# Kernel optimization log

Measured on AMD Instinct MI355X. Metric: run time of the kernel, lower is better.

## Reference

```python
import jax, jax.numpy as jnp
import numpy as np

N = 50000; E = 200000; H = 128; L = 3; T = 2; FOUT = 64
G = 1000; NP = 3; ATOM_V = 64; BOND_V = 8
EPS = 1e-5
_DEG_HIST = np.array([0., 50000., 75000., 50000., 25000.])
# PyG PNAConv: avg_deg['log'] = sum(hist[d] * log(d+1)) / num_nodes
AVG_DEG_LOG = float((np.log(np.arange(5) + 1.0) * _DEG_HIST).sum() / _DEG_HIST.sum())


def _bn(v, g, b):
    # training-mode BatchNorm1d (biased variance), eps=1e-5
    mu = v.mean(0)
    var = ((v - mu) ** 2).mean(0)
    return (v - mu) * jax.lax.rsqrt(var + EPS) * g + b


def setup_inputs() -> dict:
    key = jax.random.key(0)
    ks = jax.random.split(key, 16)
    def nrm(k, shape, fan):
        return (jax.random.normal(k, shape, dtype=jnp.float32) / np.sqrt(fan)).astype(jnp.float32)
    return {
        'x': jax.random.randint(ks[0], (N, 9), 0, ATOM_V),
        'edge_index': jax.random.randint(ks[1], (2, E), 0, N),
        'batch': jnp.sort(jax.random.randint(ks[2], (N,), 0, G)),
        'edge_attr_idx': jax.random.randint(ks[3], (E, 3), 0, BOND_V),
        'atom_emb': nrm(ks[4], (9, ATOM_V, H), H),
        'bond_emb': nrm(ks[5], (3, BOND_V, H), H),
        'edge_W': nrm(ks[6], (L, H, H), H), 'edge_b': jnp.zeros((L, H), jnp.float32),
        'pre_W': nrm(ks[7], (L, T, 3 * H, H), 3 * H), 'pre_b': jnp.zeros((L, T, H), jnp.float32),
        'post_W': nrm(ks[8], (L, T, 13 * H, FOUT), 13 * H), 'post_b': jnp.zeros((L, T, FOUT), jnp.float32),
        'lin_W': nrm(ks[9], (L, H, H), H), 'lin_b': jnp.zeros((L, H), jnp.float32),
        'bn_g': jnp.ones((L, H), jnp.float32), 'bn_b': jnp.zeros((L, H), jnp.float32),
        'mlp_W': nrm(ks[10], (2, H, H), H), 'mlp_b': jnp.zeros((2, H), jnp.float32),
        'mlp_g': jnp.ones((2, H), jnp.float32), 'mlp_be': jnp.zeros((2, H), jnp.float32),
        'hW1': nrm(ks[11], (H, H // 2), H), 'hb1': jnp.zeros((H // 2,), jnp.float32),
        'hg1': jnp.ones((H // 2,), jnp.float32), 'hbe1': jnp.zeros((H // 2,), jnp.float32),
        'hW2': nrm(ks[12], (H // 2, H // 4), H // 2), 'hb2': jnp.zeros((H // 4,), jnp.float32),
        'hg2': jnp.ones((H // 4,), jnp.float32), 'hbe2': jnp.zeros((H // 4,), jnp.float32),
        'hW3': nrm(ks[13], (H // 4, NP), H // 4), 'hb3': jnp.zeros((NP,), jnp.float32),
    }


def reference(x, edge_index, batch, edge_attr_idx, atom_emb, bond_emb,
              edge_W, edge_b, pre_W, pre_b, post_W, post_b, lin_W, lin_b,
              bn_g, bn_b, mlp_W, mlp_b, mlp_g, mlp_be,
              hW1, hb1, hg1, hbe1, hW2, hb2, hg2, hbe2, hW3, hb3):
    # encoders: sum of per-feature embeddings (OGB Atom/Bond encoder)
    h = atom_emb[jnp.arange(9), x].sum(1)               # [N,H]
    e = bond_emb[jnp.arange(3), edge_attr_idx].sum(1)   # [E,H]
    src, dst = edge_index[0], edge_index[1]
    cnt = jax.ops.segment_sum(jnp.ones((E,), jnp.float32), dst, N)
    deg = jnp.maximum(cnt, 1.0)[:, None, None]          # clamp(1), as in PyG scalers
    amp = jnp.log(deg + 1.0) / AVG_DEG_LOG
    att = AVG_DEG_LOG / jnp.log(deg + 1.0)
    has = (cnt > 0)[:, None, None]
    for l in range(L):
        ea = e @ edge_W[l] + edge_b[l]                                  # [E,H]
        msg_in = jnp.concatenate([h[dst], h[src], ea], -1)              # [E,3H]
        m = jnp.einsum('ef,tfh->eth', msg_in, pre_W[l]) + pre_b[l]      # [E,T,H]
        s1 = jax.ops.segment_sum(m, dst, N)
        s2 = jax.ops.segment_sum(m * m, dst, N)
        mean = s1 / deg
        std = jnp.sqrt(jax.nn.relu(s2 / deg - mean * mean) + EPS)
        mn = jnp.where(has, jax.ops.segment_min(m, dst, N), 0.0)
        mx = jnp.where(has, jax.ops.segment_max(m, dst, N), 0.0)
        agg = jnp.concatenate([mean, mn, mx, std], -1)                  # [N,T,4H]
        scaled = jnp.concatenate([agg, agg * amp, agg * att], -1)       # [N,T,12H]
        upd = jnp.concatenate(
            [jnp.broadcast_to(h[:, None, :], (N, T, H)), scaled], -1)   # [N,T,13H]
        o = jnp.einsum('ntf,tfo->nto', upd, post_W[l]) + post_b[l]      # [N,T,FOUT]
        o = o.reshape(N, T * FOUT) @ lin_W[l] + lin_b[l]                # [N,H]
        h = jax.nn.relu(_bn(o, bn_g[l], bn_b[l]))
    g = jax.ops.segment_sum(h, batch, G)                                # [G,H]
    for i in range(2):
        g = jax.nn.relu(_bn(g @ mlp_W[i] + mlp_b[i], mlp_g[i], mlp_be[i]))
    g = jax.nn.relu(_bn(g @ hW1 + hb1, hg1, hbe1))
    g = jax.nn.relu(_bn(g @ hW2 + hb2, hg2, hbe2))
    return g @ hW3 + hb3                                                # [G,NP]
```

## Files before the change

### kernel.cpp

```cpp
#include <hip/hip_runtime.h>
#include <math.h>


#define NN 50000
#define NE 200000
#define HD 128
#define NG 1000
#define EPSV 1e-5f
#define ALOGC 1.1330197327247628f

#define AP 1288
#define OPF 132
#define ECAP 512
#define SCB 49

typedef __bf16 bf16x8 __attribute__((ext_vector_type(8)));
typedef float f32x4 __attribute__((ext_vector_type(4)));

__device__ __forceinline__ unsigned short f2bf(float f) {
    unsigned int u = __float_as_uint(f);
    unsigned int r = (u + 0x7FFFu + ((u >> 16) & 1u)) >> 16;
    return (unsigned short)r;
}
__device__ __forceinline__ float bf2f(unsigned short h) {
    return __uint_as_float((unsigned int)h << 16);
}

__global__ void k_fill(float* __restrict__ o, float v, int n) {
    int i = blockIdx.x * 256 + threadIdx.x;
    if (i < n) o[i] = v;
}

__global__ void k_zero(float* __restrict__ z, int n) {
    int i = blockIdx.x * 256 + threadIdx.x;
    if (i < n) z[i] = 0.f;
}

__global__ __launch_bounds__(256) void k_encode_nodes(
    const int* __restrict__ x, const float* __restrict__ aemb, float* __restrict__ h) {
    __shared__ int xi[8][9];
    int nb = blockIdx.x * 8;
    int tid = threadIdx.x;
    if (tid < 72) xi[tid / 9][tid % 9] = x[nb * 9 + tid];
    __syncthreads();
    int node = tid >> 5, c4 = (tid & 31) * 4;
    float4 acc = make_float4(0.f, 0.f, 0.f, 0.f);
#pragma unroll
    for (int f = 0; f < 9; ++f) {
        float4 e = *(const float4*)(aemb + (size_t)(f * 64 + xi[node][f]) * HD + c4);
        acc.x += e.x; acc.y += e.y; acc.z += e.z; acc.w += e.w;
    }
    *(float4*)(h + (size_t)(nb + node) * HD + c4) = acc;
}

__global__ void k_count(const int* __restrict__ dst, int* __restrict__ cnt) {
    int e = blockIdx.x * 256 + threadIdx.x;
    if (e < NE) atomicAdd(&cnt[dst[e]], 1);
}

__global__ __launch_bounds__(1024) void k_scanA(const int* __restrict__ cnt,
                                                int* __restrict__ sc, int* __restrict__ tot) {
    __shared__ int buf[1024];
    int tid = threadIdx.x;
    int i = blockIdx.x * 1024 + tid;
    int v = (i < NN) ? cnt[i] : 0;
    buf[tid] = v;
    __syncthreads();
    for (int s = 1; s < 1024; s <<= 1) {
        int t = (tid >= s) ? buf[tid - s] : 0;
        __syncthreads();
        buf[tid] += t;
        __syncthreads();
    }
    if (i < NN) sc[i] = buf[tid];
    if (tid == 1023) tot[blockIdx.x] = buf[1023];
}

__global__ void k_scanB(const int* __restrict__ tot, int* __restrict__ offb) {
    if (threadIdx.x == 0) {
        int run = 0;
        for (int b = 0; b < SCB; ++b) { offb[b] = run; run += tot[b]; }
    }
}

__global__ __launch_bounds__(1024) void k_scanC(
    const int* __restrict__ cnt, const int* __restrict__ sc, const int* __restrict__ offb,
    int* __restrict__ rowptr, float* __restrict__ ampv, float* __restrict__ attv) {
    int i = blockIdx.x * 1024 + threadIdx.x;
    if (i == 0) rowptr[0] = 0;
    if (i < NN) {
        rowptr[i + 1] = offb[blockIdx.x] + sc[i];
        int v = cnt[i];
        float dg = (float)(v > 0 ? v : 1);
        float lg = logf(dg + 1.0f);
        ampv[i] = lg / ALOGC;
        attv[i] = ALOGC / lg;
    }
}

__global__ void k_scatter(const int* __restrict__ dst, const int* __restrict__ rowptr,
                          int* __restrict__ fill, int* __restrict__ eperm) {
    int e = blockIdx.x * 256 + threadIdx.x;
    if (e < NE) {
        int d = dst[e];
        int pos = rowptr[d] + atomicAdd(&fill[d], 1);
        eperm[pos] = e;
    }
}

__global__ void k_eprep(const int* __restrict__ ei, const int* __restrict__ eai,
                        const int* __restrict__ eperm, int* __restrict__ precs) {
    int p = blockIdx.x * 256 + threadIdx.x;
    if (p < NE) {
        int e = eperm[p];
        int cidx = eai[e * 3] | (eai[e * 3 + 1] << 3) | (eai[e * 3 + 2] << 6);
        precs[p] = ei[e] | (cidx << 17);
    }
}

__global__ void k_fold(const float* __restrict__ edge_W, const float* __restrict__ edge_b,
                       const float* __restrict__ pre_W, const float* __restrict__ pre_b,
                       float* __restrict__ cW, float* __restrict__ tb) {
    int l = blockIdx.y;
    int k = blockIdx.x;
    int tj = threadIdx.x;
    int t = tj >> 7, j = tj & 127;
    const float* pw = pre_W + ((size_t)(l * 2 + t) * 384 + 256) * 128 + j;
    if (k < 128) {
        const float* ew = edge_W + ((size_t)l * 128 + k) * 128;
        float acc = 0.f;
        for (int i = 0; i < 128; ++i) acc += ew[i] * pw[i * 128];
        cW[((size_t)l * 128 + k) * 256 + tj] = acc;
    } else {
        const float* eb = edge_b + l * 128;
        float acc = pre_b[(l * 2 + t) * 128 + j];
        for (int i = 0; i < 128; ++i) acc += eb[i] * pw[i * 128];
        tb[l * 256 + tj] = acc;
    }
}

__global__ void k_bond(const float* __restrict__ bemb, const float* __restrict__ cW,
                       float* __restrict__ bondc) {
    int v = blockIdx.x, f = blockIdx.y, l = blockIdx.z;
    int tj = threadIdx.x;
    const float* src = bemb + (size_t)(f * 8 + v) * 128;
    const float* w = cW + (size_t)l * 128 * 256;
    float acc = 0.f;
    for (int i = 0; i < 128; ++i) acc += src[i] * w[i * 256 + tj];
    bondc[(((size_t)l * 3 + f) * 8 + v) * 256 + tj] = acc;
}

__global__ void k_bcomb(const float* __restrict__ bondc, float* __restrict__ bcomb) {
    int ci = blockIdx.x, l = blockIdx.y, tj = threadIdx.x;
    const float* base = bondc + (size_t)l * 3 * 8 * 256;
    float v = base[((0 * 8) + (ci & 7)) * 256 + tj]
            + base[((1 * 8) + ((ci >> 3) & 7)) * 256 + tj]
            + base[((2 * 8) + (ci >> 6)) * 256 + tj];
    bcomb[((size_t)l * 512 + ci) * 256 + tj] = v;
}

__device__ __forceinline__ void pack_body2(const float* __restrict__ W, int N, int NT,
                                           unsigned short* __restrict__ pkh,
                                           unsigned short* __restrict__ pkl,
                                           int blk, int lane) {
    int kstep = blk / NT, nt = blk - kstep * NT;
    int kb = kstep * 32 + (lane >> 4) * 8;
    int col = nt * 16 + (lane & 15);
    unsigned short th[8], tl[8];
#pragma unroll
    for (int i = 0; i < 8; ++i) {
        float w = W[(size_t)(kb + i) * N + col];
        unsigned short hh = f2bf(w);
        th[i] = hh;
        tl[i] = f2bf(w - bf2f(hh));
    }
    size_t base = ((size_t)blk * 64 + lane) * 8;
    *(uint4*)(pkh + base) = *(uint4*)th;
    *(uint4*)(pkl + base) = *(uint4*)tl;
}

__global__ __launch_bounds__(64) void k_packall(
    const float* __restrict__ post_W, const float* __restrict__ lin_W,
    const float* __restrict__ pre_W,
    unsigned short* __restrict__ pkPostHi, unsigned short* __restrict__ pkPostLo,
    unsigned short* __restrict__ pkLinHi, unsigned short* __restrict__ pkLinLo,
    unsigned short* __restrict__ pkPreHi, unsigned short* __restrict__ pkPreLo) {
    int b = blockIdx.x;
    int lane = threadIdx.x;
    if (b < 1248) {
        int l = b / 416, rem = b % 416;
        int t = rem / 208, blk = rem % 208;
        size_t off = ((size_t)l * 2 + t) * 106496;
        pack_body2(post_W + ((size_t)l * 2 + t) * 1664 * 64, 64, 4,
                   pkPostHi + off, pkPostLo + off, blk, lane);
    } else if (b < 1344) {
        int idx = b - 1248;
        int l = idx / 32, blk = idx % 32;
        pack_body2(lin_W + (size_t)l * 128 * 128, 128, 8,
                   pkLinHi + (size_t)l * 16384, pkLinLo + (size_t)l * 16384, blk, lane);
    } else {
        int idx = b - 1344;
        int l = idx / 128, bb = idx % 128;
        const float* preW = pre_W + (size_t)l * 2 * 384 * 128;
        unsigned short* phi = pkPreHi + (size_t)l * 65536;
        unsigned short* plo = pkPreLo + (size_t)l * 65536;
        int kstep = bb >> 5, nt = bb & 31;
        int q = lane >> 4, nc = lane & 15;
        int col = nt * 16 + nc;
        int t = (col >> 7) & 1;
        int jcol = col & 127;
        int fbase = (col < 256) ? 0 : 128;
        unsigned short hi[8], lo[8];
#pragma unroll
        for (int i = 0; i < 8; ++i) {
            int k = kstep * 32 + q * 8 + i;
            float w = preW[((size_t)t * 384 + fbase + k) * 128 + jcol];
            unsigned short h16 = f2bf(w);
            hi[i] = h16;
            lo[i] = f2bf(w - bf2f(h16));
        }
        size_t base = ((size_t)bb * 64 + lane) * 8;
        *(uint4*)(phi + base) = *(uint4*)hi;
        *(uint4*)(plo + base) = *(uint4*)lo;
    }
}

__device__ __forceinline__ void pre_mfma_body(
    const unsigned short* __restrict__ ah, const unsigned short* __restrict__ al,
    const unsigned short* __restrict__ phi, const unsigned short* __restrict__ plo,
    const float* __restrict__ tb, int n0, int tid,
    float* __restrict__ hzd, float* __restrict__ hzs) {
    int lane = tid & 63, w = tid >> 6;
    int q = lane >> 4, nc = lane & 15;
    f32x4 acc[8];
#pragma unroll
    for (int j = 0; j < 8; ++j) acc[j] = (f32x4){0.f, 0.f, 0.f, 0.f};
#pragma unroll
    for (int kk = 0; kk < 4; ++kk) {
        bf16x8 Ahi = *(const bf16x8*)(ah + nc * 136 + kk * 32 + q * 8);
        bf16x8 Alo = *(const bf16x8*)(al + nc * 136 + kk * 32 + q * 8);
#pragma unroll
        for (int j = 0; j < 8; ++j) {
            int nt = w * 8 + j;
            size_t base = ((size_t)(kk * 32 + nt) * 64 + lane) * 8;
            bf16x8 Bhi = *(const bf16x8*)(phi + base);
            bf16x8 Blo = *(const bf16x8*)(plo + base);
            acc[j] = __builtin_amdgcn_mfma_f32_16x16x32_bf16(Ahi, Bhi, acc[j], 0, 0, 0);
            acc[j] = __builtin_amdgcn_mfma_f32_16x16x32_bf16(Ahi, Blo, acc[j], 0, 0, 0);
            acc[j] = __builtin_amdgcn_mfma_f32_16x16x32_bf16(Alo, Bhi, acc[j], 0, 0, 0);
        }
    }
#pragma unroll
    for (int j = 0; j < 8; ++j) {
        int col = (w * 8 + j) * 16 + nc;
#pragma unroll
        for (int reg = 0; reg < 4; ++reg) {
            int row = n0 + q * 4 + reg;
            if (col < 256) hzd[(size_t)row * 256 + col] = acc[j][reg] + tb[col];
            else           hzs[(size_t)row * 256 + (col - 256)] = acc[j][reg];
        }
    }
}

__global__ __launch_bounds__(256) void k_pre_m(
    const float* __restrict__ h,
    const unsigned short* __restrict__ phi, const unsigned short* __restrict__ plo,
    const float* __restrict__ tb,
    float* __restrict__ hzd, float* __restrict__ hzs) {
    __shared__ __align__(16) unsigned short ah[16 * 136];
    __shared__ __align__(16) unsigned short al[16 * 136];
    int n0 = blockIdx.x * 16;
    int tid = threadIdx.x;
    {
        int node = tid >> 4, cg = (tid & 15) * 8;
        const float* hs = h + (size_t)(n0 + node) * HD + cg;
        float4 v0 = *(const float4*)(hs);
        float4 v1 = *(const float4*)(hs + 4);
        float vv[8] = {v0.x, v0.y, v0.z, v0.w, v1.x, v1.y, v1.z, v1.w};
        unsigned short hh[8], ll[8];
#pragma unroll
        for (int i = 0; i < 8; ++i) {
            hh[i] = f2bf(vv[i]);
            ll[i] = f2bf(vv[i] - bf2f(hh[i]));
        }
        *(uint4*)(ah + node * 136 + cg) = *(uint4*)hh;
        *(uint4*)(al + node * 136 + cg) = *(uint4*)ll;
    }
    __syncthreads();
    pre_mfma_body(ah, al, phi, plo, tb, n0, tid, hzd, hzs);
}

__global__ __launch_bounds__(256) void k_bnpre(
    const float* __restrict__ o2, const float* __restrict__ stats,
    const float* __restrict__ g, const float* __restrict__ b,
    const unsigned short* __restrict__ phi, const unsigned short* __restrict__ plo,
    const float* __restrict__ tb,
    float* __restrict__ h, float* __restrict__ hzd, float* __restrict__ hzs) {
    __shared__ __align__(16) unsigned short ah[16 * 136];
    __shared__ __align__(16) unsigned short al[16 * 136];
    int n0 = blockIdx.x * 16;
    int tid = threadIdx.x;
    {
        int node = tid >> 4, cg = (tid & 15) * 8;
        int n = n0 + node;
        const float* os = o2 + (size_t)n * HD + cg;
        float4 v0 = *(const float4*)(os);
        float4 v1 = *(const float4*)(os + 4);
        float vv[8] = {v0.x, v0.y, v0.z, v0.w, v1.x, v1.y, v1.z, v1.w};
        unsigned short hh[8], ll[8];
        float ou[8];
#pragma unroll
        for (int i = 0; i < 8; ++i) {
            int c = cg + i;
            float mu = stats[c] * (1.f / NN);
            float var = stats[128 + c] * (1.f / NN) - mu * mu;
            float val = (vv[i] - mu) * rsqrtf(var + EPSV) * g[c] + b[c];
            val = fmaxf(val, 0.f);
            ou[i] = val;
            hh[i] = f2bf(val);
            ll[i] = f2bf(val - bf2f(hh[i]));
        }
        float* hd = h + (size_t)n * HD + cg;
        *(float4*)(hd) = make_float4(ou[0], ou[1], ou[2], ou[3]);
        *(float4*)(hd + 4) = make_float4(ou[4], ou[5], ou[6], ou[7]);
        *(uint4*)(ah + node * 136 + cg) = *(uint4*)hh;
        *(uint4*)(al + node * 136 + cg) = *(uint4*)ll;
    }
    __syncthreads();
    pre_mfma_body(ah, al, phi, plo, tb, n0, tid, hzd, hzs);
}

__global__ __launch_bounds__(256) void k_post(
    const float* __restrict__ h,
    const float* __restrict__ hzd, const float* __restrict__ hzs,
    const int* __restrict__ rowptr, const int* __restrict__ precs,
    const float* __restrict__ bcomb,
    const float* __restrict__ ampv, const float* __restrict__ attv,
    const unsigned short* __restrict__ pkPostHi, const unsigned short* __restrict__ pkPostLo,
    const float* __restrict__ postb,
    const unsigned short* __restrict__ pkLinHi, const unsigned short* __restrict__ pkLinLo,
    const float* __restrict__ linb,
    float* __restrict__ o2, float* __restrict__ stats) {
    __shared__ __align__(16) unsigned short a_lds[16 * AP];
    __shared__ __align__(16) float o_f[16 * OPF];
    __shared__ int es[ECAP];
    __shared__ float s_amp[16], s_att[16];
    int n0 = blockIdx.x * 16;
    int tid = threadIdx.x;

    int pbase = rowptr[n0];
    int ecount = rowptr[n0 + 16] - pbase;
    for (int i = tid; i < ecount && i < ECAP; i += 256) es[i] = precs[pbase + i];
    {
        int node = tid >> 4, cg = (tid & 15) * 8;
        const float* hs = h + (size_t)(n0 + node) * HD + cg;
        float4 v0 = *(const float4*)(hs);
        float4 v1 = *(const float4*)(hs + 4);
        unsigned short* d0 = a_lds + node * AP + cg;
        unsigned short* d1 = d0 + 640;
        unsigned short bb[8];
        bb[0] = f2bf(v0.x); bb[1] = f2bf(v0.y); bb[2] = f2bf(v0.z); bb[3] = f2bf(v0.w);
        bb[4] = f2bf(v1.x); bb[5] = f2bf(v1.y); bb[6] = f2bf(v1.z); bb[7] = f2bf(v1.w);
#pragma unroll
        for (int i = 0; i < 8; ++i) { d0[i] = bb[i]; d1[i] = bb[i]; }
    }
    if (tid < 16) { s_amp[tid] = ampv[n0 + tid]; s_att[tid] = attv[n0 + tid]; }
    __syncthreads();

    {
        int wv = tid >> 6, lane = tid & 63;
        int cc = lane * 4;
        int tt = cc >> 7, jj = cc & 127;
        bool incap = (ecount <= ECAP);
        const float4 Z4 = make_float4(0.f, 0.f, 0.f, 0.f);
        for (int i = 0; i < 4; ++i) {
            int r = wv * 4 + i;
            int n = n0 + r;
            int p0 = rowptr[n], p1 = rowptr[n + 1];
            float4 hd = *(const float4*)(hzd + (size_t)n * 256 + cc);
            float4 s1 = Z4, s2 = Z4;
            float4 mn = make_float4(3.4e38f, 3.4e38f, 3.4e38f, 3.4e38f);
            float4 mx = make_float4(-3.4e38f, -3.4e38f, -3.4e38f, -3.4e38f);
            for (int p = p0; p < p1; ++p) {
                int rec = incap ? es[p - pbase] : precs[p];
                int sp = rec & 131071;
                int ci = rec >> 17;
                float4 vs = *(const float4*)(hzs + (size_t)sp * 256 + cc);
                float4 bc = *(const float4*)(bcomb + (size_t)ci * 256 + cc);
                float wx = vs.x + bc.x, wy = vs.y + bc.y, wz = vs.z + bc.z, ww = vs.w + bc.w;
                s1.x += wx; s1.y += wy; s1.z += wz; s1.w += ww;
                s2.x += wx * wx; s2.y += wy * wy; s2.z += wz * wz; s2.w += ww * ww;
                mn.x = fminf(mn.x, wx); mn.y = fminf(mn.y, wy);
                mn.z = fminf(mn.z, wz); mn.w = fminf(mn.w, ww);
                mx.x = fmaxf(mx.x, wx); mx.y = fmaxf(mx.y, wy);
                mx.z = fmaxf(mx.z, wz); mx.w = fmaxf(mx.w, ww);
            }
            int cnt = p1 - p0;
            float inv = 1.f / (float)(cnt > 0 ? cnt : 1);
            float4 mw, stdv, mean;
            mw.x = s1.x * inv; mw.y = s1.y * inv; mw.z = s1.z * inv; mw.w = s1.w * inv;
            stdv.x = sqrtf(fmaxf(s2.x * inv - mw.x * mw.x, 0.f) + EPSV);
            stdv.y = sqrtf(fmaxf(s2.y * inv - mw.y * mw.y, 0.f) + EPSV);
            stdv.z = sqrtf(fmaxf(s2.z * inv - mw.z * mw.z, 0.f) + EPSV);
            stdv.w = sqrtf(fmaxf(s2.w * inv - mw.w * mw.w, 0.f) + EPSV);
            if (cnt > 0) {
                mean.x = hd.x + mw.x; mean.y = hd.y + mw.y;
                mean.z = hd.z + mw.z; mean.w = hd.w + mw.w;
                mn.x += hd.x; mn.y += hd.y; mn.z += hd.z; mn.w += hd.w;
                mx.x += hd.x; mx.y += hd.y; mx.z += hd.z; mx.w += hd.w;
            } else {
                mean = Z4; mn = Z4; mx = Z4;
            }
            unsigned short* d = a_lds + r * AP + tt * 640 + 128 + jj;
            d[0] = f2bf(mean.x); d[1] = f2bf(mean.y); d[2] = f2bf(mean.z); d[3] = f2bf(mean.w);
            d += 128; d[0] = f2bf(mn.x); d[1] = f2bf(mn.y); d[2] = f2bf(mn.z); d[3] = f2bf(mn.w);
            d += 128; d[0] = f2bf(mx.x); d[1] = f2bf(mx.y); d[2] = f2bf(mx.z); d[3] = f2bf(mx.w);
            d += 128; d[0] = f2bf(stdv.x); d[1] = f2bf(stdv.y); d[2] = f2bf(stdv.z); d[3] = f2bf(stdv.w);
        }
    }
    __syncthreads();

    {
        int lane = tid & 63;
        int w = tid >> 6;
        int t = w >> 1;
        int ntb = (w & 1) * 2;
        int q = lane >> 4, nc = lane & 15;
        const unsigned short* arow = a_lds + (size_t)nc * AP + t * 640 + q * 8;
        size_t toff = (size_t)t * 106496;
        const unsigned short* pkh = pkPostHi + toff;
        const unsigned short* pkl = pkPostLo + toff;
        f32x4 aP0 = {0.f, 0.f, 0.f, 0.f}, aP1 = {0.f, 0.f, 0.f, 0.f};
        f32x4 aA0 = {0.f, 0.f, 0.f, 0.f}, aA1 = {0.f, 0.f, 0.f, 0.f};
        f32x4 aT0 = {0.f, 0.f, 0.f, 0.f}, aT1 = {0.f, 0.f, 0.f, 0.f};
        for (int kk = 0; kk < 20; ++kk) {
            bf16x8 af = *(const bf16x8*)(arow + kk * 32);
            size_t ib = ((size_t)(kk * 4 + ntb) * 64 + lane) * 8;
            aP0 = __builtin_amdgcn_mfma_f32_16x16x32_bf16(af, *(const bf16x8*)(pkh + ib), aP0, 0, 0, 0);
            aP0 = __builtin_amdgcn_mfma_f32_16x16x32_bf16(af, *(const bf16x8*)(pkl + ib), aP0, 0, 0, 0);
            aP1 = __builtin_amdgcn_mfma_f32_16x16x32_bf16(af, *(const bf16x8*)(pkh + ib + 512), aP1, 0, 0, 0);
            aP1 = __builtin_amdgcn_mfma_f32_16x16x32_bf16(af, *(const bf16x8*)(pkl + ib + 512), aP1, 0, 0, 0);
            if (kk >= 4) {
                size_t ia = ((size_t)((kk + 16) * 4 + ntb) * 64 + lane) * 8;
                aA0 = __builtin_amdgcn_mfma_f32_16x16x32_bf16(af, *(const bf16x8*)(pkh + ia), aA0, 0, 0, 0);
                aA0 = __builtin_amdgcn_mfma_f32_16x16x32_bf16(af, *(const bf16x8*)(pkl + ia), aA0, 0, 0, 0);
                aA1 = __builtin_amdgcn_mfma_f32_16x16x32_bf16(af, *(const bf16x8*)(pkh + ia + 512), aA1, 0, 0, 0);
                aA1 = __builtin_amdgcn_mfma_f32_16x16x32_bf16(af, *(const bf16x8*)(pkl + ia + 512), aA1, 0, 0, 0);
                size_t it = ((size_t)((kk + 32) * 4 + ntb) * 64 + lane) * 8;
                aT0 = __builtin_amdgcn_mfma_f32_16x16x32_bf16(af, *(const bf16x8*)(pkh + it), aT0, 0, 0, 0);
                aT0 = __builtin_amdgcn_mfma_f32_16x16x32_bf16(af, *(const bf16x8*)(pkl + it), aT0, 0, 0, 0);
                aT1 = __builtin_amdgcn_mfma_f32_16x16x32_bf16(af, *(const bf16x8*)(pkh + it + 512), aT1, 0, 0, 0);
                aT1 = __builtin_amdgcn_mfma_f32_16x16x32_bf16(af, *(const bf16x8*)(pkl + it + 512), aT1, 0, 0, 0);
            }
        }
#pragma unroll
        for (int u = 0; u < 2; ++u) {
            int nt = ntb + u;
            int col = t * 64 + nt * 16 + nc;
            float pbia = postb[t * 64 + nt * 16 + nc];
            f32x4 P = u ? aP1 : aP0;
            f32x4 A = u ? aA1 : aA0;
            f32x4 T = u ? aT1 : aT0;
#pragma unroll
            for (int reg = 0; reg < 4; ++reg) {
                int mrow = q * 4 + reg;
                o_f[mrow * OPF + col] = P[reg] + s_amp[mrow] * A[reg] + s_att[mrow] * T[reg] + pbia;
            }
        }
    }
    __syncthreads();

    {
        int lane = tid & 63;
        int w = tid >> 6;
        int ntb = w * 2;
        int q = lane >> 4, nc = lane & 15;
        const float* arow = o_f + (size_t)nc * OPF + q * 8;
        f32x4 L0 = {0.f, 0.f, 0.f, 0.f}, L1 = {0.f, 0.f, 0.f, 0.f};
#pragma unroll
        for (int kk = 0; kk < 4; ++kk) {
            float4 a0 = *(const float4*)(arow + kk * 32);
            float4 a1 = *(const float4*)(arow + kk * 32 + 4);
            float vv[8] = {a0.x, a0.y, a0.z, a0.w, a1.x, a1.y, a1.z, a1.w};
            unsigned short hh[8], ll[8];
#pragma unroll
            for (int i = 0; i < 8; ++i) {
                hh[i] = f2bf(vv[i]);
                ll[i] = f2bf(vv[i] - bf2f(hh[i]));
            }
            bf16x8 Ahi = *(const bf16x8*)hh;
            bf16x8 Alo = *(const bf16x8*)ll;
            size_t ib = ((size_t)(kk * 8 + ntb) * 64 + lane) * 8;
            bf16x8 B0h = *(const bf16x8*)(pkLinHi + ib);
            bf16x8 B0l = *(const bf16x8*)(pkLinLo + ib);
            bf16x8 B1h = *(const bf16x8*)(pkLinHi + ib + 512);
            bf16x8 B1l = *(const bf16x8*)(pkLinLo + ib + 512);
            L0 = __builtin_amdgcn_mfma_f32_16x16x32_bf16(Ahi, B0h, L0, 0, 0, 0);
            L0 = __builtin_amdgcn_mfma_f32_16x16x32_bf16(Alo, B0h, L0, 0, 0, 0);
            L0 = __builtin_amdgcn_mfma_f32_16x16x32_bf16(Ahi, B0l, L0, 0, 0, 0);
            L1 = __builtin_amdgcn_mfma_f32_16x16x32_bf16(Ahi, B1h, L1, 0, 0, 0);
            L1 = __builtin_amdgcn_mfma_f32_16x16x32_bf16(Alo, B1h, L1, 0, 0, 0);
            L1 = __builtin_amdgcn_mfma_f32_16x16x32_bf16(Ahi, B1l, L1, 0, 0, 0);
        }
#pragma unroll
        for (int u = 0; u < 2; ++u) {
            int col = (ntb + u) * 16 + nc;
            float lb = linb[col];
            f32x4 L = u ? L1 : L0;
            float ps = 0.f, pss = 0.f;
#pragma unroll
            for (int reg = 0; reg < 4; ++reg) {
                int mrow = q * 4 + reg;
                float v = L[reg] + lb;
                o2[(size_t)(n0 + mrow) * HD + col] = v;
                ps += v; pss += v * v;
            }
            ps += __shfl_down(ps, 16); ps += __shfl_down(ps, 32);
            pss += __shfl_down(pss, 16); pss += __shfl_down(pss, 32);
            if (q == 0) {
                atomicAdd(&stats[col], ps);
                atomicAdd(&stats[128 + col], pss);
            }
        }
    }
}

__global__ void k_bn_relu(const float* __restrict__ o2, const float* __restrict__ stats,
                          const float* __restrict__ g, const float* __restrict__ b,
                          float* __restrict__ h) {
    int idx = blockIdx.x * 256 + threadIdx.x;
    int c = idx & 127;
    float mu = stats[c] * (1.f / NN);
    float var = stats[128 + c] * (1.f / NN) - mu * mu;
    float v = (o2[idx] - mu) * rsqrtf(var + EPSV) * g[c] + b[c];
    h[idx] = fmaxf(v, 0.f);
}

__global__ void k_pool(const float* __restrict__ h, const int* __restrict__ batch,
                       float* __restrict__ g0) {
    int c = threadIdx.x;
    int nbase = blockIdx.x * 64;
    float run = 0.f; int cur = -1;
    for (int i = 0; i < 64; ++i) {
        int n = nbase + i;
        if (n >= NN) break;
        int bb = batch[n];
        if (bb != cur) {
            if (cur >= 0) atomicAdd(&g0[(size_t)cur * HD + c], run);
            cur = bb; run = 0.f;
        }
        run += h[(size_t)n * HD + c];
    }
    if (cur >= 0) atomicAdd(&g0[(size_t)cur * HD + c], run);
}

__global__ void k_head_gemm(const float* __restrict__ x, const float* __restrict__ W,
                            const float* __restrict__ b, float* __restrict__ y,
                            float* __restrict__ stats, int K, int Kout) {
    int row = blockIdx.x;
    int col = threadIdx.x;
    if (col >= Kout) return;
    float acc = b[col];
    for (int k = 0; k < K; k += 4) {
        float4 xv = *(const float4*)(x + (size_t)row * K + k);
        acc += xv.x * W[(k + 0) * Kout + col] + xv.y * W[(k + 1) * Kout + col]
             + xv.z * W[(k + 2) * Kout + col] + xv.w * W[(k + 3) * Kout + col];
    }
    y[(size_t)row * Kout + col] = acc;
    if (stats) {
        atomicAdd(&stats[col], acc);
        atomicAdd(&stats[Kout + col], acc * acc);
    }
}

__global__ __launch_bounds__(128) void k_head_fused(
    const float* __restrict__ y_in, const float* __restrict__ stats_in,
    const float* __restrict__ g, const float* __restrict__ b,
    const float* __restrict__ W, const float* __restrict__ bias,
    float* __restrict__ y_out, float* __restrict__ stats_out, int Kin, int Kout) {
    __shared__ float row[128];
    int r = blockIdx.x, tid = threadIdx.x;
    if (tid < Kin) {
        float mu = stats_in[tid] * (1.f / NG);
        float var = stats_in[Kin + tid] * (1.f / NG) - mu * mu;
        float v = (y_in[(size_t)r * Kin + tid] - mu) * rsqrtf(var + EPSV) * g[tid] + b[tid];
        row[tid] = fmaxf(v, 0.f);
    }
    __syncthreads();
    if (tid < Kout) {
        float acc = bias[tid];
        for (int k = 0; k < Kin; ++k) acc += row[k] * W[(size_t)k * Kout + tid];
        y_out[(size_t)r * Kout + tid] = acc;
        if (stats_out) {
            atomicAdd(&stats_out[tid], acc);
            atomicAdd(&stats_out[Kout + tid], acc * acc);
        }
    }
}

extern "C" void kernel_launch(void* const* d_in, const int* in_sizes, int n_in,
                              void* d_out, int out_size, void* d_ws, size_t ws_size,
                              hipStream_t stream) {
    const int*   x        = (const int*)  d_in[0];
    const int*   ei       = (const int*)  d_in[1];
    const int*   batch    = (const int*)  d_in[2];
    const int*   eai      = (const int*)  d_in[3];
    const float* atom_emb = (const float*)d_in[4];
    const float* bond_emb = (const float*)d_in[5];
    const float* edge_W   = (const float*)d_in[6];
    const float* edge_b   = (const float*)d_in[7];
    const float* pre_W    = (const float*)d_in[8];
    const float* pre_b    = (const float*)d_in[9];
    const float* post_W   = (const float*)d_in[10];
    const float* post_b   = (const float*)d_in[11];
    const float* lin_W    = (const float*)d_in[12];
    const float* lin_b    = (const float*)d_in[13];
    const float* bn_g     = (const float*)d_in[14];
    const float* bn_b     = (const float*)d_in[15];
    const float* mlp_W    = (const float*)d_in[16];
    const float* mlp_b    = (const float*)d_in[17];
    const float* mlp_g    = (const float*)d_in[18];
    const float* mlp_be   = (const float*)d_in[19];
    const float* hW1 = (const float*)d_in[20]; const float* hb1  = (const float*)d_in[21];
    const float* hg1 = (const float*)d_in[22]; const float* hbe1 = (const float*)d_in[23];
    const float* hW2 = (const float*)d_in[24]; const float* hb2  = (const float*)d_in[25];
    const float* hg2 = (const float*)d_in[26]; const float* hbe2 = (const float*)d_in[27];
    const float* hW3 = (const float*)d_in[28]; const float* hb3  = (const float*)d_in[29];
    float* out = (float*)d_out;
    (void)n_in; (void)in_sizes;

    char* p = (char*)d_ws;
    size_t off = 0;
    auto alloc = [&](size_t bytes) -> char* {
        char* r = p + off;
        off += (bytes + 255) & ~(size_t)255;
        return r;
    };
    float* h     = (float*)alloc((size_t)NN * HD * 4);
    float* o2    = (float*)alloc((size_t)NN * HD * 4);
    float* hzd   = (float*)alloc((size_t)NN * 256 * 4);
    float* hzs   = (float*)alloc((size_t)NN * 256 * 4);
    float* ampv  = (float*)alloc((size_t)NN * 4);
    float* attv  = (float*)alloc((size_t)NN * 4);
    int*   rowptr= (int*)  alloc((size_t)(NN + 1) * 4);
    int*   eperm = (int*)  alloc((size_t)NE * 4);
    int*   precs = (int*)  alloc((size_t)NE * 4);
    int*   sc    = (int*)  alloc((size_t)NN * 4);
    int*   stot  = (int*)  alloc((size_t)SCB * 4);
    int*   soff  = (int*)  alloc((size_t)SCB * 4);
    float* cW    = (float*)alloc((size_t)3 * 128 * 256 * 4);
    float* tbb   = (float*)alloc((size_t)3 * 256 * 4);
    float* bondc = (float*)alloc((size_t)3 * 3 * 8 * 256 * 4);
    float* bcomb = (float*)alloc((size_t)3 * 512 * 256 * 4);
    unsigned short* pkPostHi = (unsigned short*)alloc((size_t)3 * 2 * 106496 * 2);
    unsigned short* pkPostLo = (unsigned short*)alloc((size_t)3 * 2 * 106496 * 2);
    unsigned short* pkLinHi  = (unsigned short*)alloc((size_t)3 * 16384 * 2);
    unsigned short* pkLinLo  = (unsigned short*)alloc((size_t)3 * 16384 * 2);
    unsigned short* pkPreHi  = (unsigned short*)alloc((size_t)3 * 65536 * 2);
    unsigned short* pkPreLo  = (unsigned short*)alloc((size_t)3 * 65536 * 2);
    float* gA    = (float*)alloc((size_t)NG * HD * 4);
    float* gB    = (float*)alloc((size_t)NG * HD * 4);
    char* z0 = p + off;
    int*   cnt   = (int*)  alloc((size_t)NN * 4);
    int*   fill  = (int*)  alloc((size_t)NN * 4);
    float* stats = (float*)alloc((size_t)3 * 256 * 4);
    float* hstats= (float*)alloc((size_t)4 * 256 * 4);
    float* g0    = (float*)alloc((size_t)NG * HD * 4);
    size_t zwords = (size_t)((p + off) - z0) / 4;

    if (off > ws_size) {
        k_fill<<<(out_size + 255) / 256, 256, 0, stream>>>(out, (float)ws_size, out_size);
        return;
    }

    k_zero<<<(int)((zwords + 255) / 256), 256, 0, stream>>>((float*)z0, (int)zwords);
    k_encode_nodes<<<NN / 8, 256, 0, stream>>>(x, atom_emb, h);
    k_count<<<(NE + 255) / 256, 256, 0, stream>>>(ei + NE, cnt);
    k_scanA<<<SCB, 1024, 0, stream>>>(cnt, sc, stot);
    k_scanB<<<1, 64, 0, stream>>>(stot, soff);
    k_scanC<<<SCB, 1024, 0, stream>>>(cnt, sc, soff, rowptr, ampv, attv);
    k_scatter<<<(NE + 255) / 256, 256, 0, stream>>>(ei + NE, rowptr, fill, eperm);
    k_eprep<<<(NE + 255) / 256, 256, 0, stream>>>(ei, eai, eperm, precs);
    k_fold<<<dim3(129, 3), 256, 0, stream>>>(edge_W, edge_b, pre_W, pre_b, cW, tbb);
    k_bond<<<dim3(8, 3, 3), 256, 0, stream>>>(bond_emb, cW, bondc);
    k_bcomb<<<dim3(512, 3), 256, 0, stream>>>(bondc, bcomb);
    k_packall<<<1728, 64, 0, stream>>>(post_W, lin_W, pre_W,
        pkPostHi, pkPostLo, pkLinHi, pkLinLo, pkPreHi, pkPreLo);

    for (int l = 0; l < 3; ++l) {
        if (l == 0) {
            k_pre_m<<<NN / 16, 256, 0, stream>>>(h, pkPreHi, pkPreLo, tbb, hzd, hzs);
        } else {
            k_bnpre<<<NN / 16, 256, 0, stream>>>(o2, stats + (l - 1) * 256,
                bn_g + (l - 1) * 128, bn_b + (l - 1) * 128,
                pkPreHi + (size_t)l * 65536, pkPreLo + (size_t)l * 65536,
                tbb + l * 256, h, hzd, hzs);
        }
        k_post<<<NN / 16, 256, 0, stream>>>(h, hzd, hzs, rowptr, precs,
            bcomb + (size_t)l * 512 * 256,
            ampv, attv,
            pkPostHi + (size_t)l * 2 * 106496, pkPostLo + (size_t)l * 2 * 106496,
            post_b + l * 2 * 64,
            pkLinHi + (size_t)l * 16384, pkLinLo + (size_t)l * 16384,
            lin_b + l * 128,
            o2, stats + l * 256);
    }
    k_bn_relu<<<(NN * HD) / 256, 256, 0, stream>>>(o2, stats + 2 * 256,
        bn_g + 2 * 128, bn_b + 2 * 128, h);

    k_pool<<<(NN + 63) / 64, 128, 0, stream>>>(h, batch, g0);

    k_head_gemm<<<NG, 128, 0, stream>>>(g0, mlp_W, mlp_b, gA, hstats, 128, 128);
    k_head_fused<<<NG, 128, 0, stream>>>(gA, hstats, mlp_g, mlp_be,
        mlp_W + 128 * 128, mlp_b + 128, gB, hstats + 256, 128, 128);
    k_head_fused<<<NG, 128, 0, stream>>>(gB, hstats + 256, mlp_g + 128, mlp_be + 128,
        hW1, hb1, gA, hstats + 512, 128, 64);
    k_head_fused<<<NG, 128, 0, stream>>>(gA, hstats + 512, hg1, hbe1,
        hW2, hb2, gB, hstats + 768, 64, 32);
    k_head_fused<<<NG, 128, 0, stream>>>(gB, hstats + 768, hg2, hbe2,
        hW3, hb3, out, (float*)nullptr, 32, 3);
}
```

Measured before the change: 981.4 us.

## Cut k_post LDS footprint by loading h fragments directly and spilling post output to global

The k_post kernel no longer stages the bf16 copy of h in shared memory. Each lane instead loads its h fragments straight from global into registers for the first four K-steps. The intermediate post-projection tile that was held in an LDS buffer (o_f) is now written to a new global scratch buffer and read back for the lin GEMM. Together these shrink LDS per block to raise occupancy, at the cost of extra global traffic. The scratch handoff also relies on writes becoming visible within the block across the existing barrier, which is a correctness risk.

```diff
diff --git a/kernel.cpp b/kernel.cpp
--- a/kernel.cpp
+++ b/kernel.cpp
@@ -9,8 +9,7 @@
 #define EPSV 1e-5f
 #define ALOGC 1.1330197327247628f
 
-#define AP 1288
-#define OPF 132
+#define APN 1032
 #define ECAP 512
 #define SCB 49
 
@@ -340,9 +339,9 @@
     const float* __restrict__ postb,
     const unsigned short* __restrict__ pkLinHi, const unsigned short* __restrict__ pkLinLo,
     const float* __restrict__ linb,
+    float* __restrict__ oSc,
     float* __restrict__ o2, float* __restrict__ stats) {
-    __shared__ __align__(16) unsigned short a_lds[16 * AP];
-    __shared__ __align__(16) float o_f[16 * OPF];
+    __shared__ __align__(16) unsigned short a_lds[16 * APN];
     __shared__ int es[ECAP];
     __shared__ float s_amp[16], s_att[16];
     int n0 = blockIdx.x * 16;
@@ -351,19 +350,6 @@
     int pbase = rowptr[n0];
     int ecount = rowptr[n0 + 16] - pbase;
     for (int i = tid; i < ecount && i < ECAP; i += 256) es[i] = precs[pbase + i];
-    {
-        int node = tid >> 4, cg = (tid & 15) * 8;
-        const float* hs = h + (size_t)(n0 + node) * HD + cg;
-        float4 v0 = *(const float4*)(hs);
-        float4 v1 = *(const float4*)(hs + 4);
-        unsigned short* d0 = a_lds + node * AP + cg;
-        unsigned short* d1 = d0 + 640;
-        unsigned short bb[8];
-        bb[0] = f2bf(v0.x); bb[1] = f2bf(v0.y); bb[2] = f2bf(v0.z); bb[3] = f2bf(v0.w);
-        bb[4] = f2bf(v1.x); bb[5] = f2bf(v1.y); bb[6] = f2bf(v1.z); bb[7] = f2bf(v1.w);
-#pragma unroll
-        for (int i = 0; i < 8; ++i) { d0[i] = bb[i]; d1[i] = bb[i]; }
-    }
     if (tid < 16) { s_amp[tid] = ampv[n0 + tid]; s_att[tid] = attv[n0 + tid]; }
     __syncthreads();
 
@@ -411,7 +397,7 @@
             } else {
                 mean = Z4; mn = Z4; mx = Z4;
             }
-            unsigned short* d = a_lds + r * AP + tt * 640 + 128 + jj;
+            unsigned short* d = a_lds + r * APN + tt * 512 + jj;
             d[0] = f2bf(mean.x); d[1] = f2bf(mean.y); d[2] = f2bf(mean.z); d[3] = f2bf(mean.w);
             d += 128; d[0] = f2bf(mn.x); d[1] = f2bf(mn.y); d[2] = f2bf(mn.z); d[3] = f2bf(mn.w);
             d += 128; d[0] = f2bf(mx.x); d[1] = f2bf(mx.y); d[2] = f2bf(mx.z); d[3] = f2bf(mx.w);
@@ -426,7 +412,19 @@
         int t = w >> 1;
         int ntb = (w & 1) * 2;
         int q = lane >> 4, nc = lane & 15;
-        const unsigned short* arow = a_lds + (size_t)nc * AP + t * 640 + q * 8;
+        bf16x8 hf[4];
+        {
+            const float* hrow = h + (size_t)(n0 + nc) * HD;
+#pragma unroll
+            for (int kk = 0; kk < 4; ++kk) {
+                float4 a0 = *(const float4*)(hrow + kk * 32 + q * 8);
+                float4 a1 = *(const float4*)(hrow + kk * 32 + q * 8 + 4);
+                unsigned short tmp[8] = {f2bf(a0.x), f2bf(a0.y), f2bf(a0.z), f2bf(a0.w),
+                                         f2bf(a1.x), f2bf(a1.y), f2bf(a1.z), f2bf(a1.w)};
+                hf[kk] = *(const bf16x8*)tmp;
+            }
+        }
+        const unsigned short* arow = a_lds + (size_t)nc * APN + t * 512 + q * 8;
         size_t toff = (size_t)t * 106496;
         const unsigned short* pkh = pkPostHi + toff;
         const unsigned short* pkl = pkPostLo + toff;
@@ -434,7 +432,7 @@
         f32x4 aA0 = {0.f, 0.f, 0.f, 0.f}, aA1 = {0.f, 0.f, 0.f, 0.f};
         f32x4 aT0 = {0.f, 0.f, 0.f, 0.f}, aT1 = {0.f, 0.f, 0.f, 0.f};
         for (int kk = 0; kk < 20; ++kk) {
-            bf16x8 af = *(const bf16x8*)(arow + kk * 32);
+            bf16x8 af = (kk < 4) ? hf[kk] : *(const bf16x8*)(arow + (kk - 4) * 32);
             size_t ib = ((size_t)(kk * 4 + ntb) * 64 + lane) * 8;
             aP0 = __builtin_amdgcn_mfma_f32_16x16x32_bf16(af, *(const bf16x8*)(pkh + ib), aP0, 0, 0, 0);
             aP0 = __builtin_amdgcn_mfma_f32_16x16x32_bf16(af, *(const bf16x8*)(pkl + ib), aP0, 0, 0, 0);
@@ -464,7 +462,8 @@
 #pragma unroll
             for (int reg = 0; reg < 4; ++reg) {
                 int mrow = q * 4 + reg;
-                o_f[mrow * OPF + col] = P[reg] + s_amp[mrow] * A[reg] + s_att[mrow] * T[reg] + pbia;
+                oSc[(size_t)(n0 + mrow) * HD + col] =
+                    P[reg] + s_amp[mrow] * A[reg] + s_att[mrow] * T[reg] + pbia;
             }
         }
     }
@@ -475,7 +474,7 @@
         int w = tid >> 6;
         int ntb = w * 2;
         int q = lane >> 4, nc = lane & 15;
-        const float* arow = o_f + (size_t)nc * OPF + q * 8;
+        const float* arow = oSc + (size_t)(n0 + nc) * HD + q * 8;
         f32x4 L0 = {0.f, 0.f, 0.f, 0.f}, L1 = {0.f, 0.f, 0.f, 0.f};
 #pragma unroll
         for (int kk = 0; kk < 4; ++kk) {
@@ -638,6 +637,7 @@
     };
     float* h     = (float*)alloc((size_t)NN * HD * 4);
     float* o2    = (float*)alloc((size_t)NN * HD * 4);
+    float* oSc   = (float*)alloc((size_t)NN * HD * 4);
     float* hzd   = (float*)alloc((size_t)NN * 256 * 4);
     float* hzs   = (float*)alloc((size_t)NN * 256 * 4);
     float* ampv  = (float*)alloc((size_t)NN * 4);
@@ -703,7 +703,7 @@
             post_b + l * 2 * 64,
             pkLinHi + (size_t)l * 16384, pkLinLo + (size_t)l * 16384,
             lin_b + l * 128,
-            o2, stats + l * 256);
+            oSc, o2, stats + l * 256);
     }
     k_bn_relu<<<(NN * HD) / 256, 256, 0, stream>>>(o2, stats + 2 * 256,
         bn_g + 2 * 128, bn_b + 2 * 128, h);
```

Measured after the change: 1.350 ms. 1.38x slower.
